# Optimization experiments

Hardware: AMD Instinct MI355X
Metric: run time of the kernel (lower is better)

## Reference

```python
import jax, jax.numpy as jnp
import numpy as np

B, IN_C, N, K, KS, OUT_C = 8, 64, 4096, 20, 20, 64
FEATS = 2 * IN_C  # conv expects in_c*2 channels; view requires feats*KS/K == 2*in_c
BN_EPS = 1e-5


def setup_inputs() -> dict:
    key = jax.random.key(0)
    k1, k2, k3, k4, k5 = jax.random.split(key, 5)
    feature = jax.random.normal(k1, (B, FEATS, N), dtype=jnp.float32)
    permatrix = jax.random.normal(k2, (B * N, K, KS), dtype=jnp.float32)
    conv_w = jax.random.normal(k3, (OUT_C, FEATS), dtype=jnp.float32)  # 1x1 Conv2d weight squeezed
    conv_b = jax.random.normal(k4, (OUT_C,), dtype=jnp.float32)
    bn_gamma = jnp.ones((OUT_C,), dtype=jnp.float32)
    bn_beta = jnp.zeros((OUT_C,), dtype=jnp.float32)
    spirals_index = jax.random.randint(k5, (B * N * K,), 0, B * N, dtype=jnp.int64)
    return {"feature": feature, "permatrix": permatrix, "conv_w": conv_w,
            "conv_b": conv_b, "bn_gamma": bn_gamma, "bn_beta": bn_beta,
            "spirals_index": spirals_index}


def reference(feature, permatrix, conv_w, conv_b, bn_gamma, bn_beta, spirals_index):
    bsize, feats, num_pts = feature.shape
    # [B, C, N] -> [B*N, C]
    flat = feature.transpose(0, 2, 1).reshape(bsize * num_pts, feats)
    # gather k spiral neighbors per point: [B*N, K, C] -> [B*N, C, K]
    spirals = flat[spirals_index].reshape(bsize * num_pts, K, feats).transpose(0, 2, 1)
    # per-point batched matmul with learned permutation matrix: [B*N, C, KS]
    spirals = jnp.einsum('pck,pks->pcs', spirals, permatrix)
    # faithful torch .view(B, N, K, -1) memory reinterpretation (C-order reshape)
    feat = spirals.reshape(bsize, num_pts, K, -1)          # [B, N, K, 2*in_c]
    x = feat.transpose(0, 3, 1, 2)                          # [B, 2*in_c, N, K]
    # 1x1 conv == channel GEMM
    y = jnp.einsum('oc,bcnk->bonk', conv_w, x) + conv_b[None, :, None, None]
    # max over neighbor dim -> [B, out_c, N]
    y = jnp.max(y, axis=-1)
    # BatchNorm1d (training mode: batch statistics over (B, N), biased var)
    mean = jnp.mean(y, axis=(0, 2), keepdims=True)
    var = jnp.mean((y - mean) ** 2, axis=(0, 2), keepdims=True)
    out = (y - mean) * jax.lax.rsqrt(var + BN_EPS)
    out = out * bn_gamma[None, :, None] + bn_beta[None, :, None]
    return out
```

## Files before the change

kernel.cpp:

```cpp
#include <hip/hip_runtime.h>
#include <hip/hip_bf16.h>

typedef short short8 __attribute__((ext_vector_type(8)));
typedef short short4v __attribute__((ext_vector_type(4)));
typedef float f32x4 __attribute__((ext_vector_type(4)));
typedef unsigned int uint2v __attribute__((ext_vector_type(2)));

#define NPTS 4096
#define BATCH 8
#define PTOT 32768
#define FEATS 128
#define KK 20
#define OUTC 64
#define PTS_PER_WAVE 16
#define WAVES 4

__device__ __forceinline__ unsigned short f2bf(float f){
  union { __hip_bfloat16 h; unsigned short u; } v;
  v.h = __hip_bfloat16(f);
  return v.u;
}

__device__ __forceinline__ void gload_lds16(const void* src, void* dst){
  __builtin_amdgcn_global_load_lds((const __attribute__((address_space(1))) void*)src,
                                   (__attribute__((address_space(3))) void*)dst, 16, 0, 0);
}

__global__ void k_transpose(const float* __restrict__ f, unsigned short* __restrict__ flat,
                            const float* __restrict__ convw, unsigned short* __restrict__ wp){
  __shared__ float tile[32][33];
  int b = blockIdx.z, c0 = blockIdx.y*32, n0 = blockIdx.x*32;
  int tx = threadIdx.x, ty = threadIdx.y;
  const float* src = f + ((size_t)b*FEATS + c0)*NPTS + n0;
  #pragma unroll
  for(int i=0;i<4;i++) tile[ty+8*i][tx] = src[(size_t)(ty+8*i)*NPTS + tx];
  if(blockIdx.z == 0 && blockIdx.y == 0 && blockIdx.x < 32){
    int e = blockIdx.x*256 + ty*32 + tx;
    int j = e & 7, l15 = (e>>3)&15, lg = (e>>7)&3, n2 = (e>>9)&3, ks = e>>11;
    int o = n2*16 + l15, c = ks*32 + lg*8 + j;
    wp[e] = f2bf(convw[o*FEATS + c]);
  }
  __syncthreads();
  unsigned short* dst = flat + ((size_t)b*NPTS + n0)*FEATS + c0;
  #pragma unroll
  for(int i=0;i<4;i++) dst[(size_t)(ty+8*i)*FEATS + tx] = f2bf(tile[tx][ty+8*i]);
}

__global__ __launch_bounds__(256, 3) void k_main(
    const unsigned short* __restrict__ flat,
    const float* __restrict__ perm_g,
    const unsigned short* __restrict__ wpack,
    const int*   __restrict__ idx_g,
    float* __restrict__ out,
    float* __restrict__ stats)
{
  const int t = threadIdx.x, lane = t & 63, w = t >> 6;
  const int l15 = lane & 15, lg = lane >> 4;

  __shared__ __align__(16) unsigned short gbuf_all[WAVES][2560];
  __shared__ __align__(16) unsigned short tbuf_all[WAVES][2560];
  __shared__ __align__(16) float pbuf_all[WAVES][2][400];
  __shared__ __align__(16) unsigned short W_lds[8192];
  __shared__ int   idx_all[WAVES][320];
  __shared__ float ybuf_all[WAVES][4*OUTC];

  unsigned short* gbuf = gbuf_all[w];
  unsigned short* tbuf = tbuf_all[w];
  int*   idxb = idx_all[w];
  float* ybuf = ybuf_all[w];
  const unsigned gbufb = (unsigned)(size_t)(const __attribute__((address_space(3))) void*)gbuf;

  const int p0 = blockIdx.x*(WAVES*PTS_PER_WAVE) + w*PTS_PER_WAVE;

  {
    const int* ib = idx_g + (size_t)p0*KK;
    #pragma unroll
    for(int it=0; it<5; it++) idxb[it*64 + lane] = ib[it*64 + lane];
  }

  #pragma unroll
  for(int it=0; it<4; it++){
    gload_lds16((const char*)wpack + it*4096 + (size_t)t*16,
                (char*)W_lds + it*4096 + w*1024);
  }
  asm volatile("s_waitcnt vmcnt(0)" ::: "memory");
  __syncthreads();

  int krowb4[5], colb[5];
  #pragma unroll
  for(int it=0; it<5; it++){
    int q = it*64 + lane;
    int cg = q/40, r = q - cg*40;
    int kgr = r>>3, rem = r&7, krem = rem>>1, chalf = rem&1;
    krowb4[it] = (kgr*4 + krem)*4;
    colb[it]   = cg*32 + chalf*16;
  }

  int kg0 = 2*lg;   if(kg0 > 4) kg0 = 0;
  int kg1 = 2*lg+1; if(kg1 > 4) kg1 = 0;
  const unsigned tra0 = gbufb + kg0*128 + l15*8;
  const unsigned tra1 = gbufb + kg1*128 + l15*8;

  const int s2 = (l15 < 4) ? (16 + l15) : 19;
  int koff[8];
  #pragma unroll
  for(int j=0;j<8;j++){ int kb = lg*160 + j*20; koff[j] = (kb > 380) ? 380 : kb; }

  float bsum[4] = {0,0,0,0}, bsq[4] = {0,0,0,0};

  #define STAGE_G(PI) do{                                                       \
    int pib_ = (PI)*80;                                                         \
    _Pragma("unroll")                                                           \
    for(int it_=0; it_<5; it_++){                                               \
      int id_ = *(const int*)((const char*)idxb + pib_ + krowb4[it_]);          \
      const char* s_ = (const char*)flat + ((size_t)(unsigned)id_*256) + colb[it_]; \
      gload_lds16(s_, (char*)gbuf + it_*1024);                                  \
    } }while(0)

  #define STAGE_P(PI) do{                                                       \
    const char* ps_ = (const char*)(perm_g + (size_t)(p0+(PI))*400);            \
    char* pd_ = (char*)&pbuf_all[w][(PI)&1][0];                                 \
    gload_lds16(ps_ + (size_t)lane*16, pd_);                                    \
    gload_lds16(ps_ + 576 + (size_t)lane*16, pd_ + 576);                        \
  }while(0)

  STAGE_G(0); STAGE_P(0); STAGE_P(1);

  const int bb = p0 >> 12, nn0 = p0 & (NPTS-1);

  for(int pi=0; pi<PTS_PER_WAVE; pi++){
    if(pi == PTS_PER_WAVE-1) asm volatile("s_waitcnt vmcnt(0)" ::: "memory");
    else                     asm volatile("s_waitcnt vmcnt(2)" ::: "memory");

    if(pi >= 4 && (pi & 3) == 0){
      float* op = out + ((size_t)bb*OUTC + lane)*NPTS + nn0 + (pi-4);
      float4 v;
      v.x = ybuf[0*64+lane]; v.y = ybuf[1*64+lane];
      v.z = ybuf[2*64+lane]; v.w = ybuf[3*64+lane];
      *(float4*)op = v;
    }

    short4v lo[8], hi[8];
    #pragma unroll
    for(int nt=0; nt<8; nt++){
      asm volatile("ds_read_b64_tr_b16 %0, %1 offset:%2" : "=v"(lo[nt]) : "v"(tra0), "i"(nt*640));
      asm volatile("ds_read_b64_tr_b16 %0, %1 offset:%2" : "=v"(hi[nt]) : "v"(tra1), "i"(nt*640));
    }
    const float* pb = &pbuf_all[w][pi&1][0];
    float p0r[8], p1r[8];
    #pragma unroll
    for(int j=0;j<8;j++){ p0r[j] = pb[koff[j]+l15]; p1r[j] = pb[koff[j]+s2]; }

    asm volatile("s_waitcnt lgkmcnt(0)" ::: "memory");
    __builtin_amdgcn_sched_barrier(0);

    if(pi+1 < PTS_PER_WAVE) STAGE_G(pi+1);
    if(pi+2 < PTS_PER_WAVE) STAGE_P(pi+2);

    short8 a0f, a1f;
    #pragma unroll
    for(int j=0;j<8;j++){
      int kk2 = lg*8 + j;
      a0f[j] = (kk2 < KK) ? (short)f2bf(p0r[j]) : (short)0;
      a1f[j] = (kk2 < KK) ? (short)f2bf(p1r[j]) : (short)0;
    }

    __builtin_amdgcn_s_setprio(1);
    #pragma unroll
    for(int nt=0; nt<8; nt++){
      short8 gf = __builtin_shufflevector(lo[nt], hi[nt], 0,1,2,3,4,5,6,7);
      f32x4 z = {0.f,0.f,0.f,0.f};
      f32x4 c0 = __builtin_amdgcn_mfma_f32_16x16x32_bf16(a0f, gf, z, 0,0,0);
      f32x4 c1 = __builtin_amdgcn_mfma_f32_16x16x32_bf16(a1f, gf, z, 0,0,0);
      const int c = nt*16 + l15;
      {
        int f0 = c*20 + lg*4;
        int byt = (f0*2) ^ (((f0>>7)&7)<<4);
        uint2v pk;
        pk.x = (unsigned)f2bf(c0[0]) | ((unsigned)f2bf(c0[1])<<16);
        pk.y = (unsigned)f2bf(c0[2]) | ((unsigned)f2bf(c0[3])<<16);
        *(uint2v*)((char*)tbuf + byt) = pk;
      }
      if(lg == 0){
        int f0 = c*20 + 16;
        int byt = (f0*2) ^ (((f0>>7)&7)<<4);
        uint2v pk;
        pk.x = (unsigned)f2bf(c1[0]) | ((unsigned)f2bf(c1[1])<<16);
        pk.y = (unsigned)f2bf(c1[2]) | ((unsigned)f2bf(c1[3])<<16);
        *(uint2v*)((char*)tbuf + byt) = pk;
      }
    }
    __builtin_amdgcn_s_setprio(0);

    f32x4 acc[2][4];
    #pragma unroll
    for(int m2=0;m2<2;m2++)
      #pragma unroll
      for(int n2=0;n2<4;n2++){ f32x4 z={0.f,0.f,0.f,0.f}; acc[m2][n2]=z; }

    const int kp1 = (l15 < 4) ? (16 + l15) : 19;
    __builtin_amdgcn_s_setprio(1);
    #pragma unroll
    for(int ks=0; ks<4; ks++){
      int a0b = (l15*256 + ks*64 + lg*16) ^ ((l15&7)<<4);
      int a1b = (kp1*256 + ks*64 + lg*16) ^ ((kp1&7)<<4);
      short8 t0 = *(const short8*)((const char*)tbuf + a0b);
      short8 t1 = *(const short8*)((const char*)tbuf + a1b);
      #pragma unroll
      for(int n2=0; n2<4; n2++){
        short8 wf = *(const short8*)((const char*)W_lds + (ks*4+n2)*1024 + lane*16);
        acc[0][n2] = __builtin_amdgcn_mfma_f32_16x16x32_bf16(t0, wf, acc[0][n2], 0,0,0);
        acc[1][n2] = __builtin_amdgcn_mfma_f32_16x16x32_bf16(t1, wf, acc[1][n2], 0,0,0);
      }
    }
    __builtin_amdgcn_s_setprio(0);

    #pragma unroll
    for(int n2=0; n2<4; n2++){
      float m0 = fmaxf(fmaxf(acc[0][n2][0], acc[0][n2][1]),
                       fmaxf(acc[0][n2][2], acc[0][n2][3]));
      float m1 = fmaxf(fmaxf(acc[1][n2][0], acc[1][n2][1]),
                       fmaxf(acc[1][n2][2], acc[1][n2][3]));
      float mm = fmaxf(m0, (lg == 0) ? m1 : -3.4e38f);
      mm = fmaxf(mm, __shfl_xor(mm, 16));
      mm = fmaxf(mm, __shfl_xor(mm, 32));
      if(lg == 0) ybuf[(pi&3)*64 + n2*16 + l15] = mm;
      bsum[n2] += mm; bsq[n2] += mm*mm;
    }
  }

  {
    float* op = out + ((size_t)bb*OUTC + lane)*NPTS + nn0 + 12;
    float4 v;
    v.x = ybuf[0*64+lane]; v.y = ybuf[1*64+lane];
    v.z = ybuf[2*64+lane]; v.w = ybuf[3*64+lane];
    *(float4*)op = v;
  }

  float* red = (float*)&idx_all[0][0];
  __syncthreads();
  if(lg == 0){
    #pragma unroll
    for(int n2=0; n2<4; n2++){
      int o = n2*16 + l15;
      red[w*128 + o]      = bsum[n2];
      red[w*128 + 64 + o] = bsq[n2];
    }
  }
  __syncthreads();
  if(w == 0){
    float s = red[lane] + red[128+lane] + red[256+lane] + red[384+lane];
    atomicAdd(&stats[lane], s);
  } else if(w == 1){
    float s = red[64+lane] + red[192+lane] + red[320+lane] + red[448+lane];
    atomicAdd(&stats[64+lane], s);
  }
}

__global__ void k_bn2(float* __restrict__ out, const float* __restrict__ stats,
                      const float* __restrict__ gamma, const float* __restrict__ beta){
  __shared__ float ss[128];
  int t = threadIdx.x;
  if(t < 64){
    float inv = 1.f/(float)PTOT;
    float mean = stats[t]*inv;
    float var  = stats[64+t]*inv - mean*mean;
    float rstd = rsqrtf(var + 1e-5f);
    float sc = gamma[t]*rstd;
    ss[t]    = sc;
    ss[64+t] = beta[t] - mean*sc;
  }
  __syncthreads();
  int i = blockIdx.x*256 + t;
  float4 v = ((float4*)out)[i];
  int o = (i >> 10) & 63;
  float sc = ss[o], sh = ss[64+o];
  v.x = v.x*sc + sh; v.y = v.y*sc + sh; v.z = v.z*sc + sh; v.w = v.w*sc + sh;
  ((float4*)out)[i] = v;
}

extern "C" void kernel_launch(void* const* d_in, const int* in_sizes, int n_in,
                              void* d_out, int out_size, void* d_ws, size_t ws_size,
                              hipStream_t stream){
  (void)in_sizes; (void)n_in; (void)ws_size;
  const float* feature    = (const float*)d_in[0];
  const float* permatrix  = (const float*)d_in[1];
  const float* conv_w     = (const float*)d_in[2];
  const float* bn_gamma   = (const float*)d_in[4];
  const float* bn_beta    = (const float*)d_in[5];
  const int*   sp_idx     = (const int*)d_in[6];
  float* out = (float*)d_out;

  unsigned short* flat  = (unsigned short*)d_ws;
  float* stats          = (float*)((char*)d_ws + (size_t)8*1024*1024);
  unsigned short* wpack = (unsigned short*)((char*)d_ws + (size_t)8*1024*1024 + 4096);

  hipMemsetAsync(stats, 0, 128*sizeof(float), stream);

  dim3 gT(NPTS/32, FEATS/32, BATCH), bT(32,8);
  k_transpose<<<gT, bT, 0, stream>>>(feature, flat, conv_w, wpack);

  k_main<<<dim3(PTOT/(WAVES*PTS_PER_WAVE)), dim3(256), 0, stream>>>(
      flat, permatrix, wpack, sp_idx, out, stats);

  k_bn2<<<dim3(out_size/4/256), dim3(256), 0, stream>>>(out, stats, bn_gamma, bn_beta);
}
```

Measured before the change: 77.09 us.

## Keep conv weights in registers and batch output stores in eight-point groups

The packed conv weight fragments now load straight from global memory into 16 short8 registers per lane, replacing the LDS staging and its block barrier, so the MFMA loop no longer issues weight LDS reads. The ybuf output staging grows from 4 to 8 points, giving two float4 stores per lane every 8 points instead of one every 4. Launch bounds drop from 3 to 2 blocks per CU to make room for the extra 64 VGPRs, trading occupancy for fewer LDS reads and less LDS use.

```diff
diff --git a/kernel.cpp b/kernel.cpp
--- a/kernel.cpp
+++ b/kernel.cpp
@@ -46,7 +46,7 @@
   for(int i=0;i<4;i++) dst[(size_t)(ty+8*i)*FEATS + tx] = f2bf(tile[tx][ty+8*i]);
 }
 
-__global__ __launch_bounds__(256, 3) void k_main(
+__global__ __launch_bounds__(256, 2) void k_main(
     const unsigned short* __restrict__ flat,
     const float* __restrict__ perm_g,
     const unsigned short* __restrict__ wpack,
@@ -60,9 +60,8 @@
   __shared__ __align__(16) unsigned short gbuf_all[WAVES][2560];
   __shared__ __align__(16) unsigned short tbuf_all[WAVES][2560];
   __shared__ __align__(16) float pbuf_all[WAVES][2][400];
-  __shared__ __align__(16) unsigned short W_lds[8192];
   __shared__ int   idx_all[WAVES][320];
-  __shared__ float ybuf_all[WAVES][4*OUTC];
+  __shared__ float ybuf_all[WAVES][8*OUTC];
 
   unsigned short* gbuf = gbuf_all[w];
   unsigned short* tbuf = tbuf_all[w];
@@ -72,19 +71,15 @@
 
   const int p0 = blockIdx.x*(WAVES*PTS_PER_WAVE) + w*PTS_PER_WAVE;
 
+  short8 wf[16];
+  #pragma unroll
+  for(int i=0; i<16; i++) wf[i] = *(const short8*)(wpack + i*512 + lane*8);
+
   {
     const int* ib = idx_g + (size_t)p0*KK;
     #pragma unroll
     for(int it=0; it<5; it++) idxb[it*64 + lane] = ib[it*64 + lane];
   }
-
-  #pragma unroll
-  for(int it=0; it<4; it++){
-    gload_lds16((const char*)wpack + it*4096 + (size_t)t*16,
-                (char*)W_lds + it*4096 + w*1024);
-  }
-  asm volatile("s_waitcnt vmcnt(0)" ::: "memory");
-  __syncthreads();
 
   int krowb4[5], colb[5];
   #pragma unroll
@@ -132,12 +127,15 @@
     if(pi == PTS_PER_WAVE-1) asm volatile("s_waitcnt vmcnt(0)" ::: "memory");
     else                     asm volatile("s_waitcnt vmcnt(2)" ::: "memory");
 
-    if(pi >= 4 && (pi & 3) == 0){
-      float* op = out + ((size_t)bb*OUTC + lane)*NPTS + nn0 + (pi-4);
-      float4 v;
-      v.x = ybuf[0*64+lane]; v.y = ybuf[1*64+lane];
-      v.z = ybuf[2*64+lane]; v.w = ybuf[3*64+lane];
-      *(float4*)op = v;
+    if(pi == 8){
+      float* op = out + ((size_t)bb*OUTC + lane)*NPTS + nn0;
+      float4 v0, v1;
+      v0.x = ybuf[0*64+lane]; v0.y = ybuf[1*64+lane];
+      v0.z = ybuf[2*64+lane]; v0.w = ybuf[3*64+lane];
+      v1.x = ybuf[4*64+lane]; v1.y = ybuf[5*64+lane];
+      v1.z = ybuf[6*64+lane]; v1.w = ybuf[7*64+lane];
+      *(float4*)op     = v0;
+      *(float4*)(op+4) = v1;
     }
 
     short4v lo[8], hi[8];
@@ -208,9 +206,8 @@
       short8 t1 = *(const short8*)((const char*)tbuf + a1b);
       #pragma unroll
       for(int n2=0; n2<4; n2++){
-        short8 wf = *(const short8*)((const char*)W_lds + (ks*4+n2)*1024 + lane*16);
-        acc[0][n2] = __builtin_amdgcn_mfma_f32_16x16x32_bf16(t0, wf, acc[0][n2], 0,0,0);
-        acc[1][n2] = __builtin_amdgcn_mfma_f32_16x16x32_bf16(t1, wf, acc[1][n2], 0,0,0);
+        acc[0][n2] = __builtin_amdgcn_mfma_f32_16x16x32_bf16(t0, wf[ks*4+n2], acc[0][n2], 0,0,0);
+        acc[1][n2] = __builtin_amdgcn_mfma_f32_16x16x32_bf16(t1, wf[ks*4+n2], acc[1][n2], 0,0,0);
       }
     }
     __builtin_amdgcn_s_setprio(0);
@@ -224,17 +221,20 @@
       float mm = fmaxf(m0, (lg == 0) ? m1 : -3.4e38f);
       mm = fmaxf(mm, __shfl_xor(mm, 16));
       mm = fmaxf(mm, __shfl_xor(mm, 32));
-      if(lg == 0) ybuf[(pi&3)*64 + n2*16 + l15] = mm;
+      if(lg == 0) ybuf[(pi&7)*64 + n2*16 + l15] = mm;
       bsum[n2] += mm; bsq[n2] += mm*mm;
     }
   }
 
   {
-    float* op = out + ((size_t)bb*OUTC + lane)*NPTS + nn0 + 12;
-    float4 v;
-    v.x = ybuf[0*64+lane]; v.y = ybuf[1*64+lane];
-    v.z = ybuf[2*64+lane]; v.w = ybuf[3*64+lane];
-    *(float4*)op = v;
+    float* op = out + ((size_t)bb*OUTC + lane)*NPTS + nn0 + 8;
+    float4 v0, v1;
+    v0.x = ybuf[0*64+lane]; v0.y = ybuf[1*64+lane];
+    v0.z = ybuf[2*64+lane]; v0.w = ybuf[3*64+lane];
+    v1.x = ybuf[4*64+lane]; v1.y = ybuf[5*64+lane];
+    v1.z = ybuf[6*64+lane]; v1.w = ybuf[7*64+lane];
+    *(float4*)op     = v0;
+    *(float4*)(op+4) = v1;
   }
 
   float* red = (float*)&idx_all[0][0];
```

Result: faster. 69.47 us (-9.9%).
